# Kernel optimization log

Hardware: AMD Instinct MI355X
Metric: run time of the kernel (lower is better)

Reference implementation:

```python
import jax, jax.numpy as jnp
import numpy as np

N_NODES = 100000
N_EDGES = 600000
N_GRAPHS = 256
K = 5
N_FEAT = 16
N_CLASSES = 4


def setup_inputs() -> dict:
    key = jax.random.key(0)
    ks = jax.random.split(key, 12)
    x = jax.random.normal(ks[0], (N_NODES, N_FEAT), dtype=jnp.float32)
    edge_index = jax.random.randint(ks[1], (2, N_EDGES), 0, N_NODES, dtype=jnp.int32)
    batch = jnp.sort(jax.random.randint(ks[2], (N_NODES,), 0, N_GRAPHS, dtype=jnp.int32))
    s = 0.1
    W11 = jax.random.normal(ks[3], (K, N_FEAT, 64), dtype=jnp.float32) * s
    b11 = jnp.zeros((64,), dtype=jnp.float32)
    W12 = jax.random.normal(ks[4], (K, N_FEAT, 64), dtype=jnp.float32) * s
    b12 = jnp.zeros((64,), dtype=jnp.float32)
    W21 = jax.random.normal(ks[5], (K, 128, 256), dtype=jnp.float32) * s
    b21 = jnp.zeros((256,), dtype=jnp.float32)
    W22 = jax.random.normal(ks[6], (K, 128, 256), dtype=jnp.float32) * s
    b22 = jnp.zeros((256,), dtype=jnp.float32)
    fc_w = jax.random.normal(ks[7], (512, N_CLASSES), dtype=jnp.float32) * s
    fc_b = jnp.zeros((N_CLASSES,), dtype=jnp.float32)
    return {
        "x": x, "edge_index": edge_index, "batch": batch,
        "W11": W11, "b11": b11, "W12": W12, "b12": b12,
        "W21": W21, "b21": b21, "W22": W22, "b22": b22,
        "fc_w": fc_w, "fc_b": fc_b,
    }


def _cheb_norm(src, dst, n_nodes):
    # PyG ChebConv (sym norm, lambda_max=2): L_hat = -D^{-1/2} A D^{-1/2},
    # zero diagonal. Degree computed over source (row) indices.
    deg = jax.ops.segment_sum(jnp.ones_like(src, dtype=jnp.float32), src,
                              num_segments=n_nodes)
    dinv = jnp.where(deg > 0, jax.lax.rsqrt(jnp.maximum(deg, 1.0)), 0.0)
    return -dinv[src] * dinv[dst]


def _cheb_conv(x, src, dst, w_norm, W, b):
    # Chebyshev recursion: Tx0=x, Tx1=L_hat x, Txk = 2 L_hat Tx_{k-1} - Tx_{k-2}
    n = x.shape[0]

    def spmm(h):  # aggregate messages from src at dst
        return jax.ops.segment_sum(h[src] * w_norm[:, None], dst, num_segments=n)

    Tx0 = x
    Tx1 = spmm(x)
    out = jnp.einsum('nf,fo->no', Tx0, W[0]) + jnp.einsum('nf,fo->no', Tx1, W[1])
    for k in range(2, W.shape[0]):
        Tx2 = 2.0 * spmm(Tx1) - Tx0
        out = out + jnp.einsum('nf,fo->no', Tx2, W[k])
        Tx0, Tx1 = Tx1, Tx2
    return out + b


def reference(x, edge_index, batch, W11, b11, W12, b12, W21, b21, W22, b22,
              fc_w, fc_b):
    src, dst = edge_index[0], edge_index[1]
    w_fwd = _cheb_norm(src, dst, N_NODES)
    w_rev = _cheb_norm(dst, src, N_NODES)  # reversed adjacency

    x1 = jax.nn.relu(_cheb_conv(x, src, dst, w_fwd, W11, b11))
    x2 = jax.nn.relu(_cheb_conv(x, dst, src, w_rev, W12, b12))
    h = jnp.concatenate([x1, x2], axis=1)  # [N, 128]

    x1 = jax.nn.relu(_cheb_conv(h, src, dst, w_fwd, W21, b21))
    x2 = jax.nn.relu(_cheb_conv(h, dst, src, w_rev, W22, b22))
    h = jnp.concatenate([x1, x2], axis=1)  # [N, 512]

    # global mean pool over graphs
    sums = jax.ops.segment_sum(h, batch, num_segments=N_GRAPHS)
    cnt = jax.ops.segment_sum(jnp.ones((h.shape[0],), dtype=h.dtype), batch,
                              num_segments=N_GRAPHS)
    pooled = sums / jnp.maximum(cnt, 1.0)[:, None]  # [G, 512]

    logits = pooled @ fc_w + fc_b
    return jax.nn.log_softmax(logits, axis=1)
```

## Files before the change

kernel.cpp:

```cpp
#include <hip/hip_runtime.h>
#include <stdint.h>

#define NNODES 100000
#define NEDGES 600000
#define NGRAPH 256
#define KCH 5
#define F1 16
#define O1 64
#define F2 128
#define O2 256
#define FT1 (KCH * F1)
#define FT2 (KCH * F2)
#define KSTEPS 20
#define KS1 3
#define LROW 40
#define NXCD 8

typedef unsigned short ushort_t;
typedef __attribute__((ext_vector_type(8))) short bf16x8;
typedef __attribute__((ext_vector_type(4))) float f32x4;

__device__ __forceinline__ float bflo(unsigned int u) {
    union { unsigned int u; float f; } v; v.u = u << 16; return v.f;
}
__device__ __forceinline__ float bfhi(unsigned int u) {
    union { unsigned int u; float f; } v; v.u = u & 0xFFFF0000u; return v.f;
}
__device__ __forceinline__ unsigned int f2bf(float f) {
    union { float f; unsigned int u; } v; v.f = f;
    return (v.u + 0x7FFFu + ((v.u >> 16) & 1u)) >> 16;
}
__device__ __forceinline__ unsigned int pack2(float lo, float hi) {
    return (f2bf(hi) << 16) | f2bf(lo);
}


__global__ void k_count(const int* __restrict__ src, const int* __restrict__ dst,
                        int* __restrict__ cntDst, int* __restrict__ cntSrc, int E) {
    int e = blockIdx.x * 256 + threadIdx.x;
    if (e < E) {
        atomicAdd(&cntDst[dst[e]], 1);
        atomicAdd(&cntSrc[src[e]], 1);
    }
}

__global__ void k_dinv(const int* __restrict__ cntDst, const int* __restrict__ cntSrc,
                       float* __restrict__ dinvF, float* __restrict__ dinvR, int n) {
    int i = blockIdx.x * 256 + threadIdx.x;
    if (i < n) {
        int cs = cntSrc[i], cd = cntDst[i];
        dinvF[i] = cs > 0 ? rsqrtf((float)cs) : 0.f;
        dinvR[i] = cd > 0 ? rsqrtf((float)cd) : 0.f;
    }
}

__global__ void k_scan1(const int* __restrict__ in, int* __restrict__ out,
                        int* __restrict__ blksum, int n) {
    __shared__ int a[512];
    __shared__ int s[256];
    int t = threadIdx.x;
    int base = blockIdx.x * 512;
    a[t]       = (base + t < n)       ? in[base + t]       : 0;
    a[t + 256] = (base + t + 256 < n) ? in[base + t + 256] : 0;
    __syncthreads();
    s[t] = a[2 * t] + a[2 * t + 1];
    __syncthreads();
    for (int off = 1; off < 256; off <<= 1) {
        int v = (t >= off) ? s[t - off] : 0;
        __syncthreads();
        s[t] += v;
        __syncthreads();
    }
    int ep = (t > 0) ? s[t - 1] : 0;
    if (base + 2 * t < n)     out[base + 2 * t]     = ep;
    if (base + 2 * t + 1 < n) out[base + 2 * t + 1] = ep + a[2 * t];
    if (t == 255) blksum[blockIdx.x] = s[255];
}

__global__ void k_scan2(int* __restrict__ blksum, int nb) {
    __shared__ int s[256];
    int t = threadIdx.x;
    s[t] = (t < nb) ? blksum[t] : 0;
    __syncthreads();
    for (int off = 1; off < 256; off <<= 1) {
        int v = (t >= off) ? s[t - off] : 0;
        __syncthreads();
        s[t] += v;
        __syncthreads();
    }
    if (t < nb) blksum[t] = (t > 0) ? s[t - 1] : 0;
}

__global__ void k_scan3(int* __restrict__ out, const int* __restrict__ blksum, int n) {
    int i = blockIdx.x * 512 + threadIdx.x;
    int add = blksum[blockIdx.x];
    if (i < n) out[i] += add;
    if (i + 256 < n) out[i + 256] += add;
}

__global__ void k_tail(int* __restrict__ off_f, int* __restrict__ off_r, int n, int E) {
    if (threadIdx.x == 0) { off_f[n] = E; off_r[n] = E; }
}

__global__ void k_scatter(const int* __restrict__ src, const int* __restrict__ dst,
                          const float* __restrict__ dinvF, const float* __restrict__ dinvR,
                          int* __restrict__ curF, int* __restrict__ curR,
                          int2* __restrict__ edF, int2* __restrict__ edR, int E,
                          int chunk) {
    int c = blockIdx.x & (NXCD - 1);
    int sb = blockIdx.x >> 3;
    int slices = gridDim.x >> 3;
    int lo = c * chunk, hi = lo + chunk;
    for (int e = sb * 256 + threadIdx.x; e < E; e += slices * 256) {
        int s = src[e], d = dst[e];
        if (d >= lo && d < hi) {
            int p = atomicAdd(&curF[d], 1);
            float wf = -dinvF[s] * dinvF[d];
            edF[p] = make_int2(s, __float_as_int(wf));
        }
        if (s >= lo && s < hi) {
            int q = atomicAdd(&curR[s], 1);
            float wr = -dinvR[s] * dinvR[d];
            edR[q] = make_int2(d, __float_as_int(wr));
        }
    }
}

__global__ void k_gstart(const int* __restrict__ batch, int* __restrict__ gstart, int n) {
    int g = blockIdx.x * 64 + threadIdx.x;
    if (g > NGRAPH) return;
    if (g == NGRAPH) { gstart[g] = n; return; }
    int lo = 0, hi = n;
    while (lo < hi) {
        int mid = (lo + hi) >> 1;
        if (batch[mid] < g) lo = mid + 1; else hi = mid;
    }
    gstart[g] = lo;
}


__global__ void k_copyx(const float* __restrict__ x, float* __restrict__ Tx, int n) {
    int tid = blockIdx.x * 256 + threadIdx.x;
    int r = tid >> 2, c = tid & 3;
    if (r < n)
        *(float4*)(Tx + (size_t)r * FT1 + c * 4) =
            *(const float4*)(x + (size_t)r * 16 + c * 4);
}

__global__ void k_spmm_f32(const float* __restrict__ Hin, float* __restrict__ Hout,
                           const float* __restrict__ Tx0,
                           const int* __restrict__ off, const int2* __restrict__ ed,
                           int n) {
    int tid = blockIdx.x * 256 + threadIdx.x;
    int r = tid >> 2, c = tid & 3;
    if (r >= n) return;
    int j0 = off[r], j1 = off[r + 1];
    float4 s = {0.f, 0.f, 0.f, 0.f};
    int j = j0;
    for (; j + 4 <= j1; j += 4) {
        int2 e0 = ed[j], e1 = ed[j + 1], e2 = ed[j + 2], e3 = ed[j + 3];
        float wa = __int_as_float(e0.y), wb = __int_as_float(e1.y);
        float wc = __int_as_float(e2.y), wd = __int_as_float(e3.y);
        const float4 h0 = *(const float4*)(Hin + (size_t)e0.x * FT1 + c * 4);
        const float4 h1 = *(const float4*)(Hin + (size_t)e1.x * FT1 + c * 4);
        const float4 h2 = *(const float4*)(Hin + (size_t)e2.x * FT1 + c * 4);
        const float4 h3 = *(const float4*)(Hin + (size_t)e3.x * FT1 + c * 4);
        s.x += wa * h0.x; s.y += wa * h0.y; s.z += wa * h0.z; s.w += wa * h0.w;
        s.x += wb * h1.x; s.y += wb * h1.y; s.z += wb * h1.z; s.w += wb * h1.w;
        s.x += wc * h2.x; s.y += wc * h2.y; s.z += wc * h2.z; s.w += wc * h2.w;
        s.x += wd * h3.x; s.y += wd * h3.y; s.z += wd * h3.z; s.w += wd * h3.w;
    }
    for (; j < j1; ++j) {
        int2 e = ed[j];
        float w2 = __int_as_float(e.y);
        const float4 h = *(const float4*)(Hin + (size_t)e.x * FT1 + c * 4);
        s.x += w2 * h.x; s.y += w2 * h.y; s.z += w2 * h.z; s.w += w2 * h.w;
    }
    float4 o;
    if (Tx0) {
        const float4 t0 = *(const float4*)(Tx0 + (size_t)r * FT1 + c * 4);
        o.x = 2.f * s.x - t0.x; o.y = 2.f * s.y - t0.y;
        o.z = 2.f * s.z - t0.z; o.w = 2.f * s.w - t0.w;
    } else {
        o = s;
    }
    *(float4*)(Hout + (size_t)r * FT1 + c * 4) = o;
}

__global__ void k_spmm_bf(const ushort_t* __restrict__ Hin, ushort_t* __restrict__ Hout,
                          const ushort_t* __restrict__ Tx0,
                          const int* __restrict__ off, const int2* __restrict__ ed,
                          int n) {
    int r = blockIdx.x * 4 + (threadIdx.x >> 6);
    r = __builtin_amdgcn_readfirstlane(r);
    int c = threadIdx.x & 63;
    if (r >= n) return;
    int j0 = __builtin_amdgcn_readfirstlane(off[r]);
    int j1 = __builtin_amdgcn_readfirstlane(off[r + 1]);
    float s0 = 0.f, s1 = 0.f;
    for (int j = j0; j < j1; j += 8) {
        float w[8];
        unsigned int h[8];
#pragma unroll
        for (int sl = 0; sl < 8; ++sl) {
            int jj = j + sl;
            int jc = jj < j1 ? jj : j1 - 1;
            int2 e = ed[jc];
            w[sl] = (jj < j1) ? __int_as_float(e.y) : 0.f;
            h[sl] = *(const unsigned int*)(Hin + (size_t)e.x * FT2 + c * 2);
        }
#pragma unroll
        for (int sl = 0; sl < 8; ++sl) {
            s0 = fmaf(bflo(h[sl]), w[sl], s0);
            s1 = fmaf(bfhi(h[sl]), w[sl], s1);
        }
    }
    if (Tx0) {
        unsigned int t0 = *(const unsigned int*)(Tx0 + (size_t)r * FT2 + c * 2);
        s0 = 2.f * s0 - bflo(t0);
        s1 = 2.f * s1 - bfhi(t0);
    }
    *(unsigned int*)(Hout + (size_t)r * FT2 + c * 2) = pack2(s0, s1);
}

__global__ void k_packW1(const float* __restrict__ W, ushort_t* __restrict__ Bp) {
    int tid = blockIdx.x * 256 + threadIdx.x;
    if (tid >= 4 * KS1 * 64) return;
    int lane = tid & 63;
    int ks = (tid >> 6) % KS1;
    int nt = tid / (64 * KS1);
    int k0 = ks * 32 + (lane >> 4) * 8;
    int ncol = nt * 16 + (lane & 15);
    float v[8];
#pragma unroll
    for (int j = 0; j < 8; ++j) {
        int k = k0 + j;
        v[j] = (k < FT1) ? W[(size_t)k * O1 + ncol] : 0.f;
    }
    uint4 o;
    o.x = pack2(v[0], v[1]); o.y = pack2(v[2], v[3]);
    o.z = pack2(v[4], v[5]); o.w = pack2(v[6], v[7]);
    *(uint4*)(Bp + (size_t)tid * 8) = o;
}

__global__ __launch_bounds__(256) void k_gemm1_mfma(
    const float* __restrict__ A, const ushort_t* __restrict__ Bp,
    const float* __restrict__ bias, ushort_t* __restrict__ out, int n) {
    int lane = threadIdx.x & 63;
    int wvi = threadIdx.x >> 6;
    int mrow = lane & 15;
    int quad = lane >> 4;
    int m0w = blockIdx.x * 64 + wvi * 16;
    int row = m0w + mrow;
    int rowc = row < n ? row : n - 1;
    const float* Ar = A + (size_t)rowc * FT1 + quad * 8;

    f32x4 acc[4] = {};
#pragma unroll
    for (int ks = 0; ks < KS1; ++ks) {
        float4 a0 = *(const float4*)(Ar + ks * 32);
        float4 a1 = *(const float4*)(Ar + ks * 32 + 4);
        union { bf16x8 v; unsigned int u[4]; } ua;
        ua.u[0] = pack2(a0.x, a0.y);
        ua.u[1] = pack2(a0.z, a0.w);
        ua.u[2] = pack2(a1.x, a1.y);
        ua.u[3] = pack2(a1.z, a1.w);
#pragma unroll
        for (int nf = 0; nf < 4; ++nf) {
            bf16x8 bfr = *(const bf16x8*)(Bp + ((size_t)(nf * KS1 + ks) * 64 + lane) * 8);
            acc[nf] = __builtin_amdgcn_mfma_f32_16x16x32_bf16(ua.v, bfr, acc[nf], 0, 0, 0);
        }
    }
#pragma unroll
    for (int nf = 0; nf < 4; ++nf) {
        float bb = bias[nf * 16 + mrow];
#pragma unroll
        for (int reg = 0; reg < 4; ++reg) {
            int orow = m0w + quad * 4 + reg;
            if (orow < n)
                out[(size_t)orow * FT2 + nf * 16 + mrow] =
                    (ushort_t)f2bf(fmaxf(acc[nf][reg] + bb, 0.f));
        }
    }
}

__global__ void k_packW(const float* __restrict__ W, ushort_t* __restrict__ Bp) {
    int tid = blockIdx.x * 256 + threadIdx.x;
    if (tid >= 16 * KSTEPS * 64) return;
    int lane = tid & 63;
    int ks = (tid >> 6) % KSTEPS;
    int nt = tid / (64 * KSTEPS);
    int k0 = ks * 32 + (lane >> 4) * 8;
    int ncol = nt * 16 + (lane & 15);
    float v[8];
#pragma unroll
    for (int j = 0; j < 8; ++j) v[j] = W[(size_t)(k0 + j) * O2 + ncol];
    uint4 o;
    o.x = pack2(v[0], v[1]); o.y = pack2(v[2], v[3]);
    o.z = pack2(v[4], v[5]); o.w = pack2(v[6], v[7]);
    *(uint4*)(Bp + (size_t)tid * 8) = o;
}

__global__ __launch_bounds__(256) void k_gemm2_mfma(
    const ushort_t* __restrict__ A, const ushort_t* __restrict__ Bp,
    const float* __restrict__ bias, float* __restrict__ pooled, int colofs,
    const int* __restrict__ batch, int n) {
    __shared__ ushort_t lds[2][64 * LROW];

    int lane = threadIdx.x & 63;
    int wv = threadIdx.x >> 6;
    int m0 = blockIdx.x * 64;
    int mrow = lane & 15;
    int quad = lane >> 4;
    int srow = threadIdx.x >> 2;
    int sc = threadIdx.x & 3;

    const ushort_t* Ag = A + (size_t)(m0 + srow) * FT2 + sc * 8;
    const ushort_t* Bbase = Bp + ((size_t)(wv * 4) * KSTEPS * 64 + lane) * 8;
    int sidx = srow * LROW + sc * 8;

    f32x4 acc[4][4] = {};

    uint4 nxt;
    bf16x8 bcur[4], bnxt[4];
    {
        uint4 c0 = *(const uint4*)(Ag);
        *(uint4*)&lds[0][sidx] = c0;
        nxt = *(const uint4*)(Ag + 32);
#pragma unroll
        for (int nf = 0; nf < 4; ++nf)
            bcur[nf] = *(const bf16x8*)(Bbase + ((size_t)nf * KSTEPS) * 64 * 8);
    }

    for (int ks = 0; ks < KSTEPS; ++ks) {
        __syncthreads();
        if (ks + 1 < KSTEPS)
            *(uint4*)&lds[(ks + 1) & 1][sidx] = nxt;
        if (ks + 2 < KSTEPS)
            nxt = *(const uint4*)(Ag + (ks + 2) * 32);
        if (ks + 1 < KSTEPS) {
#pragma unroll
            for (int nf = 0; nf < 4; ++nf)
                bnxt[nf] = *(const bf16x8*)(Bbase + ((size_t)nf * KSTEPS + ks + 1) * 64 * 8);
        }
        bf16x8 af[4];
        const ushort_t* lbuf = &lds[ks & 1][0];
#pragma unroll
        for (int mf = 0; mf < 4; ++mf)
            af[mf] = *(const bf16x8*)(lbuf + (mf * 16 + mrow) * LROW + quad * 8);
#pragma unroll
        for (int mf = 0; mf < 4; ++mf)
#pragma unroll
            for (int nf = 0; nf < 4; ++nf)
                acc[mf][nf] = __builtin_amdgcn_mfma_f32_16x16x32_bf16(
                    af[mf], bcur[nf], acc[mf][nf], 0, 0, 0);
#pragma unroll
        for (int nf = 0; nf < 4; ++nf) bcur[nf] = bnxt[nf];
    }

    float bcol[4];
#pragma unroll
    for (int nf = 0; nf < 4; ++nf) bcol[nf] = bias[wv * 64 + nf * 16 + mrow];

#pragma unroll
    for (int mf = 0; mf < 4; ++mf) {
        int t0 = m0 + mf * 16;
        if (t0 >= n) break;
        int te = (t0 + 15 < n) ? t0 + 15 : n - 1;
        int r0 = t0 + quad * 4;
        if (batch[t0] == batch[te]) {
            int g = batch[t0];
#pragma unroll
            for (int nf = 0; nf < 4; ++nf) {
                float s = 0.f;
#pragma unroll
                for (int reg = 0; reg < 4; ++reg) {
                    float v = fmaxf(acc[mf][nf][reg] + bcol[nf], 0.f);
                    if (r0 + reg < n) s += v;
                }
                s += __shfl_xor(s, 16, 64);
                s += __shfl_xor(s, 32, 64);
                if (quad == 0)
                    atomicAdd(pooled + (size_t)g * 512 + colofs + wv * 64 + nf * 16 + mrow, s);
            }
        } else {
            int gb[4];
#pragma unroll
            for (int reg = 0; reg < 4; ++reg)
                gb[reg] = batch[(r0 + reg < n) ? r0 + reg : n - 1];
#pragma unroll
            for (int nf = 0; nf < 4; ++nf) {
                int col = colofs + wv * 64 + nf * 16 + mrow;
                float run = 0.f;
                int g = gb[0];
                bool any = false;
#pragma unroll
                for (int reg = 0; reg < 4; ++reg) {
                    int row = r0 + reg;
                    if (row >= n) break;
                    float v = fmaxf(acc[mf][nf][reg] + bcol[nf], 0.f);
                    if (gb[reg] != g) {
                        atomicAdd(pooled + (size_t)g * 512 + col, run);
                        run = 0.f;
                        g = gb[reg];
                    }
                    run += v;
                    any = true;
                }
                if (any) atomicAdd(pooled + (size_t)g * 512 + col, run);
            }
        }
    }
}

__global__ void k_logits(const float* __restrict__ pooled, const int* __restrict__ gstart,
                         const float* __restrict__ fcw, const float* __restrict__ fcb,
                         float* __restrict__ out) {
    int g = threadIdx.x;
    int cnt = gstart[g + 1] - gstart[g];
    float inv = 1.f / (float)(cnt > 1 ? cnt : 1);
    float lg[4];
#pragma unroll
    for (int o = 0; o < 4; ++o) lg[o] = fcb[o];
    for (int f = 0; f < 512; ++f) {
        float p = pooled[g * 512 + f] * inv;
#pragma unroll
        for (int o = 0; o < 4; ++o) lg[o] = fmaf(p, fcw[f * 4 + o], lg[o]);
    }
    float m = fmaxf(fmaxf(lg[0], lg[1]), fmaxf(lg[2], lg[3]));
    float s = 0.f;
#pragma unroll
    for (int o = 0; o < 4; ++o) s += expf(lg[o] - m);
    float l = logf(s);
#pragma unroll
    for (int o = 0; o < 4; ++o) out[g * 4 + o] = lg[o] - m - l;
}


extern "C" void kernel_launch(void* const* d_in, const int* in_sizes, int n_in,
                              void* d_out, int out_size, void* d_ws, size_t ws_size,
                              hipStream_t stream) {
    const float* x   = (const float*)d_in[0];
    const int* ei    = (const int*)d_in[1];
    const int* batch = (const int*)d_in[2];
    const float* W11 = (const float*)d_in[3];
    const float* b11 = (const float*)d_in[4];
    const float* W12 = (const float*)d_in[5];
    const float* b12 = (const float*)d_in[6];
    const float* W21 = (const float*)d_in[7];
    const float* b21 = (const float*)d_in[8];
    const float* W22 = (const float*)d_in[9];
    const float* b22 = (const float*)d_in[10];
    const float* fcw = (const float*)d_in[11];
    const float* fcb = (const float*)d_in[12];
    float* out = (float*)d_out;

    const int N = in_sizes[0] / F1;
    const int E = in_sizes[1] / 2;
    const int* src = ei;
    const int* dst = ei + E;

    char* w = (char*)d_ws;
    size_t pos = 0;
    auto alloc = [&](size_t bytes) -> void* {
        void* p = w + pos;
        pos += (bytes + 255) & ~(size_t)255;
        return p;
    };
    int* cur_f   = (int*)alloc((size_t)N * 4);
    int* cur_r   = (int*)alloc((size_t)N * 4);
    int* off_f   = (int*)alloc((size_t)(N + 1) * 4);
    int* off_r   = (int*)alloc((size_t)(N + 1) * 4);
    float* dinvF = (float*)alloc((size_t)N * 4);
    float* dinvR = (float*)alloc((size_t)N * 4);
    int2* ed_f   = (int2*)alloc((size_t)E * 8);
    int2* ed_r   = (int2*)alloc((size_t)E * 8);
    int* blks_f  = (int*)alloc(1024);
    int* blks_r  = (int*)alloc(1024);
    int* gstart  = (int*)alloc((NGRAPH + 1) * 4);
    float* pooled = (float*)alloc((size_t)NGRAPH * 512 * 4);
    ushort_t* BpF = (ushort_t*)alloc((size_t)FT2 * O2 * 2);
    ushort_t* BpR = (ushort_t*)alloc((size_t)FT2 * O2 * 2);
    ushort_t* Bp1F = (ushort_t*)alloc((size_t)4 * KS1 * 64 * 8 * 2);
    ushort_t* Bp1R = (ushort_t*)alloc((size_t)4 * KS1 * 64 * 8 * 2);
    float* TxAll1 = (float*)alloc(((size_t)N * FT1 + 256) * 4);
    ushort_t* TxAll2 = (ushort_t*)alloc((size_t)(N + 64) * FT2 * 2);

    (void)hipMemsetAsync(cur_f, 0, (size_t)N * 4, stream);
    (void)hipMemsetAsync(cur_r, 0, (size_t)N * 4, stream);
    (void)hipMemsetAsync(pooled, 0, (size_t)NGRAPH * 512 * 4, stream);

    int gE = (E + 255) / 256, gN = (N + 255) / 256;
    k_count<<<gE, 256, 0, stream>>>(src, dst, cur_f, cur_r, E);
    k_dinv<<<gN, 256, 0, stream>>>(cur_f, cur_r, dinvF, dinvR, N);

    int NB = (N + 511) / 512;
    k_scan1<<<NB, 256, 0, stream>>>(cur_f, off_f, blks_f, N);
    k_scan1<<<NB, 256, 0, stream>>>(cur_r, off_r, blks_r, N);
    k_scan2<<<1, 256, 0, stream>>>(blks_f, NB);
    k_scan2<<<1, 256, 0, stream>>>(blks_r, NB);
    k_scan3<<<NB, 256, 0, stream>>>(off_f, blks_f, N);
    k_scan3<<<NB, 256, 0, stream>>>(off_r, blks_r, N);
    k_tail<<<1, 64, 0, stream>>>(off_f, off_r, N, E);
    (void)hipMemcpyAsync(cur_f, off_f, (size_t)N * 4, hipMemcpyDeviceToDevice, stream);
    (void)hipMemcpyAsync(cur_r, off_r, (size_t)N * 4, hipMemcpyDeviceToDevice, stream);
    int chunk = (N + NXCD - 1) / NXCD;
    k_scatter<<<NXCD * 256, 256, 0, stream>>>(src, dst, dinvF, dinvR, cur_f, cur_r,
                                              ed_f, ed_r, E, chunk);
    k_gstart<<<5, 64, 0, stream>>>(batch, gstart, N);
    k_packW<<<80, 256, 0, stream>>>(W21, BpF);
    k_packW<<<80, 256, 0, stream>>>(W22, BpR);
    k_packW1<<<3, 256, 0, stream>>>(W11, Bp1F);
    k_packW1<<<3, 256, 0, stream>>>(W12, Bp1R);

    k_copyx<<<(N * 4 + 255) / 256, 256, 0, stream>>>(x, TxAll1, N);
    int gs1 = (N * 4 + 255) / 256;
    int gg1 = (N + 63) / 64;
    auto C1 = [&](int k) { return TxAll1 + k * F1; };
    k_spmm_f32<<<gs1, 256, 0, stream>>>(C1(0), C1(1), nullptr, off_f, ed_f, N);
    k_spmm_f32<<<gs1, 256, 0, stream>>>(C1(1), C1(2), C1(0), off_f, ed_f, N);
    k_spmm_f32<<<gs1, 256, 0, stream>>>(C1(2), C1(3), C1(1), off_f, ed_f, N);
    k_spmm_f32<<<gs1, 256, 0, stream>>>(C1(3), C1(4), C1(2), off_f, ed_f, N);
    k_gemm1_mfma<<<gg1, 256, 0, stream>>>(TxAll1, Bp1F, b11, TxAll2, N);
    k_spmm_f32<<<gs1, 256, 0, stream>>>(C1(0), C1(1), nullptr, off_r, ed_r, N);
    k_spmm_f32<<<gs1, 256, 0, stream>>>(C1(1), C1(2), C1(0), off_r, ed_r, N);
    k_spmm_f32<<<gs1, 256, 0, stream>>>(C1(2), C1(3), C1(1), off_r, ed_r, N);
    k_spmm_f32<<<gs1, 256, 0, stream>>>(C1(3), C1(4), C1(2), off_r, ed_r, N);
    k_gemm1_mfma<<<gg1, 256, 0, stream>>>(TxAll1, Bp1R, b12, TxAll2 + O1, N);

    int gs2 = (N + 3) / 4;
    auto C2 = [&](int k) { return TxAll2 + k * F2; };
    int gg = (N + 63) / 64;
    k_spmm_bf<<<gs2, 256, 0, stream>>>(C2(0), C2(1), nullptr, off_f, ed_f, N);
    k_spmm_bf<<<gs2, 256, 0, stream>>>(C2(1), C2(2), C2(0), off_f, ed_f, N);
    k_spmm_bf<<<gs2, 256, 0, stream>>>(C2(2), C2(3), C2(1), off_f, ed_f, N);
    k_spmm_bf<<<gs2, 256, 0, stream>>>(C2(3), C2(4), C2(2), off_f, ed_f, N);
    k_gemm2_mfma<<<gg, 256, 0, stream>>>(TxAll2, BpF, b21, pooled, 0, batch, N);
    k_spmm_bf<<<gs2, 256, 0, stream>>>(C2(0), C2(1), nullptr, off_r, ed_r, N);
    k_spmm_bf<<<gs2, 256, 0, stream>>>(C2(1), C2(2), C2(0), off_r, ed_r, N);
    k_spmm_bf<<<gs2, 256, 0, stream>>>(C2(2), C2(3), C2(1), off_r, ed_r, N);
    k_spmm_bf<<<gs2, 256, 0, stream>>>(C2(3), C2(4), C2(2), off_r, ed_r, N);
    k_gemm2_mfma<<<gg, 256, 0, stream>>>(TxAll2, BpR, b22, pooled, 256, batch, N);

    k_logits<<<1, 256, 0, stream>>>(pooled, gstart, fcw, fcb, out);
}
```

Before: 744.2 us.

## Load GEMM A fragments directly from global and split SpMM tail loop

The layer-2 MFMA GEMM no longer stages A tiles through double-buffered LDS with block barriers. Each wave now loads its own A fragments straight from global memory into registers, prefetching one step ahead, with row indices clamped to n. This removes the LDS traffic and __syncthreads, but every wave now re-reads the same A rows (four times redundant global/L2 traffic) and uses more registers. The bf16 SpMM also gets a branch-free main loop over full groups of 8 edges plus a separate masked remainder step.

```diff
diff --git a/kernel.cpp b/kernel.cpp
--- a/kernel.cpp
+++ b/kernel.cpp
@@ -13,7 +13,6 @@
 #define FT2 (KCH * F2)
 #define KSTEPS 20
 #define KS1 3
-#define LROW 40
 #define NXCD 8
 
 typedef unsigned short ushort_t;
@@ -198,16 +197,35 @@
     int j0 = __builtin_amdgcn_readfirstlane(off[r]);
     int j1 = __builtin_amdgcn_readfirstlane(off[r + 1]);
     float s0 = 0.f, s1 = 0.f;
-    for (int j = j0; j < j1; j += 8) {
+    int j = j0;
+    int jfull = j0 + ((j1 - j0) & ~7);
+    for (; j < jfull; j += 8) {
         float w[8];
         unsigned int h[8];
 #pragma unroll
         for (int sl = 0; sl < 8; ++sl) {
-            int jj = j + sl;
-            int jc = jj < j1 ? jj : j1 - 1;
-            int2 e = ed[jc];
-            w[sl] = (jj < j1) ? __int_as_float(e.y) : 0.f;
+            int2 e = ed[j + sl];
+            w[sl] = __int_as_float(e.y);
             h[sl] = *(const unsigned int*)(Hin + (size_t)e.x * FT2 + c * 2);
+        }
+#pragma unroll
+        for (int sl = 0; sl < 8; ++sl) {
+            s0 = fmaf(bflo(h[sl]), w[sl], s0);
+            s1 = fmaf(bfhi(h[sl]), w[sl], s1);
+        }
+    }
+    int rem = j1 - j;
+    if (rem) {
+        float w[8];
+        unsigned int h[8];
+#pragma unroll
+        for (int sl = 0; sl < 8; ++sl) {
+            w[sl] = 0.f; h[sl] = 0u;
+            if (sl < rem) {
+                int2 e = ed[j + sl];
+                w[sl] = __int_as_float(e.y);
+                h[sl] = *(const unsigned int*)(Hin + (size_t)e.x * FT2 + c * 2);
+            }
         }
 #pragma unroll
         for (int sl = 0; sl < 8; ++sl) {
@@ -305,55 +323,47 @@
     const ushort_t* __restrict__ A, const ushort_t* __restrict__ Bp,
     const float* __restrict__ bias, float* __restrict__ pooled, int colofs,
     const int* __restrict__ batch, int n) {
-    __shared__ ushort_t lds[2][64 * LROW];
-
     int lane = threadIdx.x & 63;
     int wv = threadIdx.x >> 6;
     int m0 = blockIdx.x * 64;
     int mrow = lane & 15;
     int quad = lane >> 4;
-    int srow = threadIdx.x >> 2;
-    int sc = threadIdx.x & 3;
-
-    const ushort_t* Ag = A + (size_t)(m0 + srow) * FT2 + sc * 8;
+
+    const ushort_t* Abase[4];
+#pragma unroll
+    for (int mf = 0; mf < 4; ++mf) {
+        int row = m0 + mf * 16 + mrow;
+        int rowc = row < n ? row : n - 1;
+        Abase[mf] = A + (size_t)rowc * FT2 + quad * 8;
+    }
     const ushort_t* Bbase = Bp + ((size_t)(wv * 4) * KSTEPS * 64 + lane) * 8;
-    int sidx = srow * LROW + sc * 8;
 
     f32x4 acc[4][4] = {};
-
-    uint4 nxt;
-    bf16x8 bcur[4], bnxt[4];
-    {
-        uint4 c0 = *(const uint4*)(Ag);
-        *(uint4*)&lds[0][sidx] = c0;
-        nxt = *(const uint4*)(Ag + 32);
-#pragma unroll
-        for (int nf = 0; nf < 4; ++nf)
-            bcur[nf] = *(const bf16x8*)(Bbase + ((size_t)nf * KSTEPS) * 64 * 8);
-    }
-
+    bf16x8 acur[4], bcur[4], anxt[4], bnxt[4];
+#pragma unroll
+    for (int mf = 0; mf < 4; ++mf) acur[mf] = *(const bf16x8*)(Abase[mf]);
+#pragma unroll
+    for (int nf = 0; nf < 4; ++nf)
+        bcur[nf] = *(const bf16x8*)(Bbase + ((size_t)nf * KSTEPS) * 512);
+
+#pragma unroll 2
     for (int ks = 0; ks < KSTEPS; ++ks) {
-        __syncthreads();
-        if (ks + 1 < KSTEPS)
-            *(uint4*)&lds[(ks + 1) & 1][sidx] = nxt;
-        if (ks + 2 < KSTEPS)
-            nxt = *(const uint4*)(Ag + (ks + 2) * 32);
         if (ks + 1 < KSTEPS) {
 #pragma unroll
+            for (int mf = 0; mf < 4; ++mf)
+                anxt[mf] = *(const bf16x8*)(Abase[mf] + (ks + 1) * 32);
+#pragma unroll
             for (int nf = 0; nf < 4; ++nf)
-                bnxt[nf] = *(const bf16x8*)(Bbase + ((size_t)nf * KSTEPS + ks + 1) * 64 * 8);
-        }
-        bf16x8 af[4];
-        const ushort_t* lbuf = &lds[ks & 1][0];
-#pragma unroll
-        for (int mf = 0; mf < 4; ++mf)
-            af[mf] = *(const bf16x8*)(lbuf + (mf * 16 + mrow) * LROW + quad * 8);
+                bnxt[nf] = *(const bf16x8*)(Bbase + ((size_t)nf * KSTEPS + ks + 1) * 512);
+        }
 #pragma unroll
         for (int mf = 0; mf < 4; ++mf)
 #pragma unroll
             for (int nf = 0; nf < 4; ++nf)
                 acc[mf][nf] = __builtin_amdgcn_mfma_f32_16x16x32_bf16(
-                    af[mf], bcur[nf], acc[mf][nf], 0, 0, 0);
+                    acur[mf], bcur[nf], acc[mf][nf], 0, 0, 0);
+#pragma unroll
+        for (int mf = 0; mf < 4; ++mf) acur[mf] = anxt[mf];
 #pragma unroll
         for (int nf = 0; nf < 4; ++nf) bcur[nf] = bnxt[nf];
     }
```

Measured after the change: 864.6 us. 1.16x slower.
